# Kernel optimization log

Measured on AMD Instinct MI355X. Metric: run time of the kernel, lower is better.

The kernel has to match this reference:

```python
import jax, jax.numpy as jnp
import numpy as np

P, B, NB, NC = 256, 16, 1024, 37
L = 24  # max pairs per image == torch.mode-count for sorted im_idx (matches counts in setup_inputs)
DREL = 1936


def _linear(x, w, b):
    return x @ w.T + b


def _conv(x, w, b, stride, pad):
    y = jax.lax.conv_general_dilated(x, w, (stride, stride), [(pad, pad), (pad, pad)],
                                     dimension_numbers=('NCHW', 'OIHW', 'NCHW'))
    return y + b[None, :, None, None]


def _bn(x, g, bt, m, v):
    # eval-mode BatchNorm2d, eps=1e-5
    return g[None, :, None, None] * (x - m[None, :, None, None]) * jax.lax.rsqrt(v[None, :, None, None] + 1e-5) + bt[None, :, None, None]


def setup_inputs() -> dict:
    key = jax.random.key(0)
    ks = jax.random.split(key, 24)
    counts = np.concatenate([np.full(8, 8), np.full(8, 24)])  # sums to P=256, max = L = 24
    im_idx = jnp.asarray(np.repeat(np.arange(B), counts), dtype=jnp.int32)
    s = 0.02
    return {
        'features': jax.random.normal(ks[0], (NB, 2048), jnp.float32),
        'pair_idx': jax.random.randint(ks[1], (P, 2), 0, NB, jnp.int32),
        'im_idx': im_idx,
        'labels': jax.random.randint(ks[2], (NB,), 0, NC, jnp.int32),
        'union_feat': jax.random.normal(ks[3], (P, 1024, 7, 7), jnp.float32),
        'spatial_masks': jax.random.uniform(ks[4], (P, 2, 27, 27), jnp.float32),
        'w_union': jax.random.normal(ks[5], (256, 1024), jnp.float32) * s,
        'b_union': jnp.zeros((256,), jnp.float32),
        'conv1_w': jax.random.normal(ks[6], (128, 2, 7, 7), jnp.float32) * 0.05,
        'conv1_b': jnp.zeros((128,), jnp.float32),
        'bn1_g': jnp.ones((128,), jnp.float32),
        'bn1_b': jnp.zeros((128,), jnp.float32),
        'bn1_m': jnp.zeros((128,), jnp.float32),
        'bn1_v': jnp.ones((128,), jnp.float32),
        'conv2_w': jax.random.normal(ks[7], (256, 128, 3, 3), jnp.float32) * 0.05,
        'conv2_b': jnp.zeros((256,), jnp.float32),
        'bn2_g': jnp.ones((256,), jnp.float32),
        'bn2_b': jnp.zeros((256,), jnp.float32),
        'bn2_m': jnp.zeros((256,), jnp.float32),
        'bn2_v': jnp.ones((256,), jnp.float32),
        'subj_w': jax.random.normal(ks[8], (512, 2048), jnp.float32) * s,
        'subj_b': jnp.zeros((512,), jnp.float32),
        'obj_w': jax.random.normal(ks[9], (512, 2048), jnp.float32) * s,
        'obj_b': jnp.zeros((512,), jnp.float32),
        'vr_w': jax.random.normal(ks[10], (512, 12544), jnp.float32) * s,
        'vr_b': jnp.zeros((512,), jnp.float32),
        'emb1': jax.random.normal(ks[11], (NC, 200), jnp.float32),
        'emb2': jax.random.normal(ks[12], (NC, 200), jnp.float32),
        'bil_w': jax.random.normal(ks[13], (712, 712, 712), jnp.float32) * (1.0 / 712.0),
        'bil_b': jnp.zeros((712,), jnp.float32),
        'lin_w': jax.random.normal(ks[14], (712, 1424), jnp.float32) * s,
        'lin_b': jnp.zeros((712,), jnp.float32),
        'proj_w': jax.random.normal(ks[15], (1424, 1424), jnp.float32) * s,
        'proj_b': jnp.zeros((1424,), jnp.float32),
        'ac_w': jax.random.normal(ks[16], (157, 1936), jnp.float32) * s,
        'ac_b': jnp.zeros((157,), jnp.float32),
    }


def reference(features, pair_idx, im_idx, labels, union_feat, spatial_masks,
              w_union, b_union, conv1_w, conv1_b, bn1_g, bn1_b, bn1_m, bn1_v,
              conv2_w, conv2_b, bn2_g, bn2_b, bn2_m, bn2_v,
              subj_w, subj_b, obj_w, obj_b, vr_w, vr_b, emb1, emb2,
              bil_w, bil_b, lin_w, lin_b, proj_w, proj_b, ac_w, ac_b):
    # ragged gathers over pairs
    subj_rep = _linear(features[pair_idx[:, 0]], subj_w, subj_b)  # [P,512]
    obj_rep = _linear(features[pair_idx[:, 1]], obj_w, obj_b)    # [P,512]

    # union_func1 is a 1x1 conv -> channel contraction
    u = jnp.einsum('nchw,oc->nohw', union_feat, w_union) + b_union[None, :, None, None]
    x = jax.nn.relu(_conv(spatial_masks, conv1_w, conv1_b, 2, 3))        # [P,128,14,14]
    x = _bn(x, bn1_g, bn1_b, bn1_m, bn1_v)
    x = jax.lax.reduce_window(x, -jnp.inf, jax.lax.max, (1, 1, 3, 3), (1, 1, 2, 2),
                              ((0, 0), (0, 0), (1, 1), (1, 1)))          # [P,128,7,7]
    x = jax.nn.relu(_conv(x, conv2_w, conv2_b, 1, 1))                    # [P,256,7,7]
    x = _bn(x, bn2_g, bn2_b, bn2_m, bn2_v)
    vr = _linear((u + x).reshape(P, 256 * 49), vr_w, vr_b)               # [P,512]

    s = jnp.concatenate([subj_rep, emb1[labels[pair_idx[:, 0]]]], axis=1)  # [P,712]
    o = jnp.concatenate([obj_rep, emb2[labels[pair_idx[:, 1]]]], axis=1)   # [P,712]

    # nn.Bilinear over all pairs at once (per-row op, so the per-image loop vectorizes away)
    bil = jnp.einsum('nh,oht,nt->no', s, bil_w, o) + bil_b               # [P,712]
    z = _linear(jnp.concatenate([s, o], axis=1), lin_w, lin_b)           # [P,712]
    z = _linear(jax.nn.relu(jnp.concatenate([z, bil], axis=1)), proj_w, proj_b)  # [P,1424]
    rel = jnp.concatenate([z, vr], axis=1)                               # [P,1936]

    counts = jax.ops.segment_sum(jnp.ones((P,), jnp.int32), im_idx, num_segments=B)
    pooled = jax.ops.segment_max(rel, im_idx, num_segments=B)            # pool_type='max'
    starts = jnp.cumsum(counts) - counts
    pos = jnp.arange(P, dtype=jnp.int32) - starts[im_idx]                # position within image group
    memory = jnp.zeros((L, B, DREL), rel.dtype).at[pos, im_idx].set(rel)
    mask = (jnp.arange(L)[None, :] >= counts[:, None]).astype(jnp.uint8)  # [B,L]

    act = jax.nn.sigmoid(_linear(pooled, ac_w, ac_b))                    # [B,157]
    return act, pooled, memory, mask
```

## Files before the change

kernel.cpp:

```cpp
#include <hip/hip_runtime.h>
#include <math.h>

#define DEV __device__ __forceinline__

#define PP    256
#define BIMG  16
#define HB    712
#define KBIL  (712*712)
#define KSTEPS (KBIL/32)
#define DRELC 1936
#define BSPLIT 16
#define ZPB    991
#define KC     16
#define SLDS   520

#define SZ_ACT    (16*157)
#define OFF_ACT   0
#define OFF_POOLED (SZ_ACT)
#define SZ_POOLED (16*1936)
#define OFF_MEM   (OFF_POOLED + SZ_POOLED)
#define SZ_MEM    (24*16*1936)
#define OFF_MASK  (OFF_MEM + SZ_MEM)
#define SZ_MASK   (16*24)

#define OFF_S     0
#define OFF_O     (OFF_S + 256*712)
#define OFF_Z1    (OFF_O + 256*712)
#define OFF_BIL   (OFF_Z1 + 256*712)
#define OFF_REL   (OFF_BIL + 256*712)
#define OFF_UBUF  (OFF_REL + 256*1936)
#define OFF_XP    (OFF_UBUF + 12544*256)
#define OFF_SHARED (OFF_XP + 256*128*49)
#define OFF_X1    OFF_SHARED
#define OFF_PVR   OFF_SHARED
#define OFF_PBIL  OFF_UBUF
#define OFF_PLIN  OFF_UBUF
#define OFF_PPROJ OFF_UBUF
#define SZ_SHARED (256*128*196)
#define OFF_INTS  (OFF_SHARED + SZ_SHARED)
#define OFF_OB    (OFF_INTS + 256)
#define OFF_ST    (OFF_OB + 91136)

typedef __bf16 bf16x4 __attribute__((ext_vector_type(4)));
typedef __bf16 bf16x8 __attribute__((ext_vector_type(8)));
typedef float  f32x4  __attribute__((ext_vector_type(4)));

__global__ __launch_bounds__(256) void prep_k(const float* __restrict__ s,
    const float* __restrict__ o, __bf16* __restrict__ ob, float* __restrict__ sT) {
  int i = blockIdx.x*256 + threadIdx.x;
  if (i < 256*712) {
    ob[i] = (__bf16)o[i];
  } else {
    int j = i - 256*712;
    if (j < 712*256) {
      int h = j >> 8, n = j & 255;
      sT[j] = s[n*712 + h];
    }
  }
}

__global__ __launch_bounds__(256, 3) void bil_mfma_k(
    const __bf16* __restrict__ ob, const float* __restrict__ sT,
    const float* __restrict__ W, float* __restrict__ part) {
  __shared__ __align__(16) __bf16 Wsh[2][16*SLDS];

  const int tid = threadIdx.x;
  const int wv = tid >> 6, lane = tid & 63;
  const int lr = lane & 15, lg = lane >> 4;
  const int c0 = blockIdx.x * 16;
  const int bz = blockIdx.y;
  const int zbase = bz * ZPB;
  const int zcntT = min(ZPB, KSTEPS - zbase);
  const int nrounds = (zcntT + KC - 1) / KC;

  const int srow = tid >> 4;
  const int sl = tid & 15;
  const int scol = min(c0 + srow, 711);
  const float* wrow = W + (size_t)scol * KBIL;

  const int n0 = wv * 64;
  const int myc = c0 + lr;

  f32x4 acc[4];
  #pragma unroll
  for (int rf = 0; rf < 4; rf++) { acc[rf][0]=0.f; acc[rf][1]=0.f; acc[rf][2]=0.f; acc[rf][3]=0.f; }

  float4 st0, st1, st2, st3, st4, st5, st6, st7;
  auto stage_load = [&](int r) {
    const int kb = (zbase + r*KC) * 32 + sl*4;
    #define LD(J, DST) { int k = kb + (J)*64; if (k > KBIL-4) k = KBIL-4; \
                         DST = *(const float4*)(wrow + k); }
    LD(0, st0) LD(1, st1) LD(2, st2) LD(3, st3)
    LD(4, st4) LD(5, st5) LD(6, st6) LD(7, st7)
    #undef LD
  };
  auto stage_store = [&](int buf) {
    __bf16* base = &Wsh[buf][srow*SLDS + sl*4];
    #define ST(J, SRC) { bf16x4 b; b[0]=(__bf16)SRC.x; b[1]=(__bf16)SRC.y; \
                         b[2]=(__bf16)SRC.z; b[3]=(__bf16)SRC.w; \
                         *(bf16x4*)(base + (J)*64) = b; }
    ST(0, st0) ST(1, st1) ST(2, st2) ST(3, st3)
    ST(4, st4) ST(5, st5) ST(6, st6) ST(7, st7)
    #undef ST
  };

  stage_load(0);
  stage_store(0);
  if (nrounds > 1) stage_load(1);
  __syncthreads();

  for (int r = 0; r < nrounds; ++r) {
    const int zr0 = zbase + r*KC;
    const int zc = min(KC, zbase + zcntT - zr0);
    const int buf = r & 1;
    for (int zs = 0; zs < zc; ++zs) {
      bf16x8 b8 = *(const bf16x8*)&Wsh[buf][lr*SLDS + zs*32 + lg*8];
      const int kk = (zr0 + zs)*32 + lg*8;
      const int h = kk / 712;
      const int t = kk - h*712;
      #pragma unroll
      for (int rf = 0; rf < 4; rf++) {
        const int n = n0 + rf*16 + lr;
        bf16x8 o8 = *(const bf16x8*)&ob[(size_t)n*712 + t];
        const float sv = sT[h*256 + n];
        bf16x8 a8;
        #pragma unroll
        for (int i = 0; i < 8; i++) a8[i] = (__bf16)(sv * (float)o8[i]);
        acc[rf] = __builtin_amdgcn_mfma_f32_16x16x32_bf16(a8, b8, acc[rf], 0, 0, 0);
      }
    }
    if (r + 1 < nrounds) {
      stage_store((r+1)&1);
      __syncthreads();
      if (r + 2 < nrounds) stage_load(r+2);
    }
  }

  if (myc < 712) {
    #pragma unroll
    for (int rf = 0; rf < 4; rf++) {
      #pragma unroll
      for (int i = 0; i < 4; i++) {
        const int n = n0 + rf*16 + lg*4 + i;
        part[((size_t)bz*256 + n)*712 + myc] = acc[rf][i];
      }
    }
  }
}

struct GP {
  const float* A; const float* A2; const float* B; const float* bias;
  float* C;
  const int* gidx; int goff;
  int M, N, K;
  int ldc, coff;
  int kChunk;
  const float* bn_g; const float* bn_b; const float* bn_m; const float* bn_v;
  const float* B2; const float* bias2; float* C2;
};


template<int MODE>
DEV float loadA(const GP& p, int r, int k) {
  if (MODE == 0) { int fr = p.gidx[2*r + (int)blockIdx.z]; return p.A[fr*2048 + k]; }
  if (MODE == 2 || MODE == 8) return p.A[r*p.K + k];
  if (MODE == 3) return (k < 712) ? p.A[r*712 + k] : p.A2[r*712 + (k-712)];
  if (MODE == 4) { float v = (k < 712) ? p.A[r*712 + k] : p.A2[r*712 + (k-712)];
                   return fmaxf(v, 0.f); }
  if (MODE == 5) { int n = r/49, q = r - n*49; return p.A[(n*1024 + k)*49 + q]; }
  if (MODE == 6) {
    int n = r/49, q = r - n*49; int py = q/7, px = q - py*7;
    int ic = k/9, k9 = k - ic*9; int dy = k9/3, dx = k9 - dy*3;
    int iy = py + dy - 1, ix = px + dx - 1;
    if ((unsigned)iy >= 7u || (unsigned)ix >= 7u) return 0.f;
    return p.A[(n*128 + ic)*49 + iy*7 + ix];
  }
  return 0.f;
}

template<int MODE>
DEV float loadB(const GP& p, int c, int k) {
  if (MODE == 0) { const float* Bp = blockIdx.z ? p.B2 : p.B; return Bp[c*p.K + k]; }
  return p.B[c*p.K + k];
}

template<int MODE>
__global__ __launch_bounds__(256) void gemm_k(GP p) {
  __shared__ __align__(16) __bf16 Ash[2][64*44];
  __shared__ __align__(16) __bf16 Bsh[2][64*44];
  const int tid = threadIdx.x;
  const int srow = tid & 63, koff = (tid >> 6) * 8;
  const int col0 = blockIdx.x * 64, row0 = blockIdx.y * 64;
  const int kStart = (MODE == 0) ? 0 : blockIdx.z * p.kChunk;
  const int kEnd = min(p.K, kStart + p.kChunk);
  const int wv = tid >> 6, lane = tid & 63;
  const int lr = lane & 15, lg = lane >> 4;
  const int rh = wv >> 1, ch = wv & 1;

  f32x4 acc[2][2];
  #pragma unroll
  for (int a = 0; a < 2; a++)
    #pragma unroll
    for (int b = 0; b < 2; b++) { acc[a][b][0]=0.f; acc[a][b][1]=0.f; acc[a][b][2]=0.f; acc[a][b][3]=0.f; }

  for (int kb = kStart; kb < kEnd; kb += 32) {
    {
      const int gr = row0 + srow;
      float v[8];
      #pragma unroll
      for (int i = 0; i < 8; i++) {
        const int gk = kb + koff + i;
        v[i] = (gr < p.M && gk < kEnd) ? loadA<MODE>(p, gr, gk) : 0.f;
      }
      bf16x8 hi, lo;
      #pragma unroll
      for (int i = 0; i < 8; i++) {
        __bf16 h = (__bf16)v[i];
        hi[i] = h;
        lo[i] = (__bf16)(v[i] - (float)h);
      }
      *(bf16x8*)&Ash[0][srow*44 + koff] = hi;
      *(bf16x8*)&Ash[1][srow*44 + koff] = lo;
    }
    {
      const int gc = col0 + srow;
      float v[8];
      #pragma unroll
      for (int i = 0; i < 8; i++) {
        const int gk = kb + koff + i;
        v[i] = (gc < p.N && gk < kEnd) ? loadB<MODE>(p, gc, gk) : 0.f;
      }
      bf16x8 hi, lo;
      #pragma unroll
      for (int i = 0; i < 8; i++) {
        __bf16 h = (__bf16)v[i];
        hi[i] = h;
        lo[i] = (__bf16)(v[i] - (float)h);
      }
      *(bf16x8*)&Bsh[0][srow*44 + koff] = hi;
      *(bf16x8*)&Bsh[1][srow*44 + koff] = lo;
    }
    __syncthreads();
    #pragma unroll
    for (int rf = 0; rf < 2; rf++) {
      bf16x8 ahi = *(const bf16x8*)&Ash[0][(rh*32 + rf*16 + lr)*44 + lg*8];
      bf16x8 alo = *(const bf16x8*)&Ash[1][(rh*32 + rf*16 + lr)*44 + lg*8];
      #pragma unroll
      for (int cf = 0; cf < 2; cf++) {
        bf16x8 bhi = *(const bf16x8*)&Bsh[0][(ch*32 + cf*16 + lr)*44 + lg*8];
        bf16x8 blo = *(const bf16x8*)&Bsh[1][(ch*32 + cf*16 + lr)*44 + lg*8];
        acc[rf][cf] = __builtin_amdgcn_mfma_f32_16x16x32_bf16(ahi, bhi, acc[rf][cf], 0, 0, 0);
        acc[rf][cf] = __builtin_amdgcn_mfma_f32_16x16x32_bf16(ahi, blo, acc[rf][cf], 0, 0, 0);
        acc[rf][cf] = __builtin_amdgcn_mfma_f32_16x16x32_bf16(alo, bhi, acc[rf][cf], 0, 0, 0);
      }
    }
    __syncthreads();
  }

  #pragma unroll
  for (int rf = 0; rf < 2; rf++) {
    #pragma unroll
    for (int cf = 0; cf < 2; cf++) {
      const int c = col0 + ch*32 + cf*16 + lr;
      if (c >= p.N) continue;
      #pragma unroll
      for (int i = 0; i < 4; i++) {
        const int r = row0 + rh*32 + rf*16 + lg*4 + i;
        if (r >= p.M) continue;
        float v = acc[rf][cf][i];
        if (MODE == 2 || MODE == 3 || MODE == 4) {
          p.C[(size_t)blockIdx.z * p.M * p.N + (size_t)r * p.N + c] = v;
        } else if (MODE == 5) {
          int n = r/49, q = r - n*49;
          p.C[n*12544 + c*49 + q] = v + p.bias[c];
        } else if (MODE == 6) {
          int n = r/49, q = r - n*49;
          float sc = p.bn_g[c] / sqrtf(p.bn_v[c] + 1e-5f);
          float sh = p.bn_b[c] - p.bn_m[c]*sc;
          float t2 = fmaxf(v + p.bias[c], 0.f)*sc + sh;
          p.C[n*12544 + c*49 + q] += t2;
        } else if (MODE == 8) {
          float t2 = v + p.bias[c];
          p.C[r*p.ldc + p.coff + c] = 1.f/(1.f + expf(-t2));
        } else {
          const float* bb = blockIdx.z ? p.bias2 : p.bias;
          float* Cp = blockIdx.z ? p.C2 : p.C;
          Cp[r*p.ldc + p.coff + c] = v + bb[c];
        }
      }
    }
  }
}

__global__ __launch_bounds__(256) void reduce_k(const float* __restrict__ part,
    const float* __restrict__ bias, float* __restrict__ out,
    int S, int MN, int N, int ldc, int coff) {
  int i = blockIdx.x*256 + threadIdx.x;
  if (i >= MN) return;
  float s = 0.f;
  for (int z = 0; z < S; z++) s += part[(size_t)z*MN + i];
  int r = i / N, c = i - r*N;
  out[r*ldc + coff + c] = s + bias[c];
}

__global__ __launch_bounds__(256) void emb_k(const int* __restrict__ pi,
    const int* __restrict__ labels, const float* __restrict__ e1,
    const float* __restrict__ e2, float* __restrict__ s, float* __restrict__ o) {
  int i = blockIdx.x*256 + threadIdx.x;
  if (i >= 2*256*200) return;
  int which = i / (256*200); int rest = i - which*(256*200);
  int n = rest / 200; int j = rest - n*200;
  int lab = labels[pi[2*n + which]];
  float v = which ? e2[lab*200 + j] : e1[lab*200 + j];
  (which ? o : s)[n*712 + 512 + j] = v;
}

__global__ __launch_bounds__(256) void conv1_k(const float* __restrict__ in,
    const float* __restrict__ w, const float* __restrict__ bias,
    const float* __restrict__ g, const float* __restrict__ bt,
    const float* __restrict__ m, const float* __restrict__ vv,
    float* __restrict__ out) {
  int idx = blockIdx.x*256 + threadIdx.x;
  if (idx >= 256*128*14) return;
  int oy = idx % 14; int t = idx / 14; int c = t & 127; int n = t >> 7;
  float acc[14];
  float b0 = bias[c];
  #pragma unroll
  for (int ox = 0; ox < 14; ox++) acc[ox] = b0;
  for (int ci = 0; ci < 2; ci++) {
    #pragma unroll
    for (int ky = 0; ky < 7; ky++) {
      int iy = oy*2 - 3 + ky;
      if ((unsigned)iy >= 27u) continue;
      const float* ir = in + ((n*2 + ci)*27 + iy)*27;
      const float* wr = w + ((c*2 + ci)*7 + ky)*7;
      float iv[27];
      #pragma unroll
      for (int x = 0; x < 27; x++) iv[x] = ir[x];
      float wk[7];
      #pragma unroll
      for (int kx = 0; kx < 7; kx++) wk[kx] = wr[kx];
      #pragma unroll
      for (int kx = 0; kx < 7; kx++)
        #pragma unroll
        for (int ox = 0; ox < 14; ox++) {
          int ix = ox*2 - 3 + kx;
          if (ix >= 0 && ix < 27) acc[ox] += iv[ix]*wk[kx];
        }
    }
  }
  float sc = g[c] / sqrtf(vv[c] + 1e-5f);
  float sh = bt[c] - m[c]*sc;
  float* orow = out + ((n*128 + c)*14 + oy)*14;
  #pragma unroll
  for (int ox = 0; ox < 14; ox++) orow[ox] = fmaxf(acc[ox], 0.f)*sc + sh;
}

__global__ __launch_bounds__(256) void pool_k(const float* __restrict__ x1,
                                              float* __restrict__ xp) {
  int idx = blockIdx.x*256 + threadIdx.x;
  if (idx >= 256*128*49) return;
  int px = idx % 7; int t = idx / 7; int py = t % 7; t /= 7;
  int c = t & 127; int n = t >> 7;
  float mx = -INFINITY;
  for (int dy = 0; dy < 3; dy++) {
    int y = py*2 - 1 + dy;
    if ((unsigned)y >= 14u) continue;
    for (int dx = 0; dx < 3; dx++) {
      int x = px*2 - 1 + dx;
      if ((unsigned)x >= 14u) continue;
      mx = fmaxf(mx, x1[((n*128 + c)*14 + y)*14 + x]);
    }
  }
  xp[((n*128 + c)*7 + py)*7 + px] = mx;
}

__global__ __launch_bounds__(256) void seg_k(const int* __restrict__ im,
    int* __restrict__ counts, int* __restrict__ starts, int* __restrict__ pos) {
  __shared__ int c[16], s[16];
  int tid = threadIdx.x;
  if (tid < 16) c[tid] = 0;
  __syncthreads();
  atomicAdd(&c[im[tid]], 1);
  __syncthreads();
  if (tid == 0) { int run = 0; for (int b = 0; b < 16; b++) { s[b] = run; run += c[b]; } }
  __syncthreads();
  if (tid < 16) { counts[tid] = c[tid]; starts[tid] = s[tid]; }
  pos[tid] = tid - s[im[tid]];
}

__global__ __launch_bounds__(256) void zeromask_k(float* __restrict__ out,
                                                  const int* __restrict__ counts) {
  int i = blockIdx.x*256 + threadIdx.x;
  if (i < SZ_MEM) { out[OFF_MEM + i] = 0.f; return; }
  int j = i - SZ_MEM;
  if (j < SZ_MASK) {
    int b = j / 24, l = j - b*24;
    out[OFF_MASK + j] = (l >= counts[b]) ? 1.f : 0.f;
  }
}

__global__ __launch_bounds__(256) void scatter_k(const float* __restrict__ rel,
    const int* __restrict__ pos, const int* __restrict__ im, float* __restrict__ out) {
  int n = blockIdx.x;
  int l = pos[n], b = im[n];
  float* dst = out + OFF_MEM + ((size_t)l*16 + b)*1936;
  const float* src = rel + (size_t)n*1936;
  for (int d = threadIdx.x; d < 1936; d += 256) dst[d] = src[d];
}

__global__ __launch_bounds__(256) void pooled_k(const float* __restrict__ rel,
    const int* __restrict__ starts, const int* __restrict__ counts,
    float* __restrict__ out) {
  int b = blockIdx.y;
  int d = blockIdx.x*256 + threadIdx.x;
  if (d >= 1936) return;
  int st = starts[b], ct = counts[b];
  float mx = -INFINITY;
  for (int i = 0; i < ct; i++) mx = fmaxf(mx, rel[(size_t)(st + i)*1936 + d]);
  out[OFF_POOLED + b*1936 + d] = mx;
}

extern "C" void kernel_launch(void* const* d_in, const int* in_sizes, int n_in,
                              void* d_out, int out_size, void* d_ws, size_t ws_size,
                              hipStream_t stream) {
  const float* features   = (const float*)d_in[0];
  const int*   pair_idx   = (const int*)d_in[1];
  const int*   im_idx     = (const int*)d_in[2];
  const int*   labels     = (const int*)d_in[3];
  const float* union_feat = (const float*)d_in[4];
  const float* spatial    = (const float*)d_in[5];
  const float* w_union    = (const float*)d_in[6];
  const float* b_union    = (const float*)d_in[7];
  const float* conv1_w    = (const float*)d_in[8];
  const float* conv1_b    = (const float*)d_in[9];
  const float* bn1_g      = (const float*)d_in[10];
  const float* bn1_b      = (const float*)d_in[11];
  const float* bn1_m      = (const float*)d_in[12];
  const float* bn1_v      = (const float*)d_in[13];
  const float* conv2_w    = (const float*)d_in[14];
  const float* conv2_b    = (const float*)d_in[15];
  const float* bn2_g      = (const float*)d_in[16];
  const float* bn2_b      = (const float*)d_in[17];
  const float* bn2_m      = (const float*)d_in[18];
  const float* bn2_v      = (const float*)d_in[19];
  const float* subj_w     = (const float*)d_in[20];
  const float* subj_b     = (const float*)d_in[21];
  const float* obj_w      = (const float*)d_in[22];
  const float* obj_b      = (const float*)d_in[23];
  const float* vr_w       = (const float*)d_in[24];
  const float* vr_b       = (const float*)d_in[25];
  const float* emb1       = (const float*)d_in[26];
  const float* emb2       = (const float*)d_in[27];
  const float* bil_w      = (const float*)d_in[28];
  const float* bil_b      = (const float*)d_in[29];
  const float* lin_w      = (const float*)d_in[30];
  const float* lin_b      = (const float*)d_in[31];
  const float* proj_w     = (const float*)d_in[32];
  const float* proj_b     = (const float*)d_in[33];
  const float* ac_w       = (const float*)d_in[34];
  const float* ac_b       = (const float*)d_in[35];

  float* ws = (float*)d_ws;
  float* s_mat  = ws + OFF_S;
  float* o_mat  = ws + OFF_O;
  float* z1     = ws + OFF_Z1;
  float* bilbuf = ws + OFF_BIL;
  float* rel    = ws + OFF_REL;
  float* ubuf   = ws + OFF_UBUF;
  float* x1     = ws + OFF_X1;
  float* xp     = ws + OFF_XP;
  float* pvr    = ws + OFF_PVR;
  float* pbil   = ws + OFF_PBIL;
  float* plin   = ws + OFF_PLIN;
  float* pproj  = ws + OFF_PPROJ;
  int*   ints   = (int*)(ws + OFF_INTS);
  __bf16* obp   = (__bf16*)(ws + OFF_OB);
  float* sTp    = ws + OFF_ST;
  int* counts = ints; int* starts = ints + 16; int* pos = ints + 32;
  float* out = (float*)d_out;

  dim3 blk(256);

  {
    GP g{}; g.A = features; g.gidx = pair_idx;
    g.B = subj_w;  g.bias = subj_b;  g.C = s_mat;
    g.B2 = obj_w;  g.bias2 = obj_b;  g.C2 = o_mat;
    g.M = 256; g.N = 512; g.K = 2048; g.ldc = 712; g.coff = 0; g.kChunk = 2048;
    gemm_k<0><<<dim3(8,4,2), blk, 0, stream>>>(g);
  }
  emb_k<<<dim3(400), blk, 0, stream>>>(pair_idx, labels, emb1, emb2, s_mat, o_mat);

  {
    GP g{}; g.A = union_feat; g.B = w_union; g.bias = b_union; g.C = ubuf;
    g.M = 12544; g.N = 256; g.K = 1024; g.kChunk = 1024;
    gemm_k<5><<<dim3(4,196,1), blk, 0, stream>>>(g);
  }

  conv1_k<<<dim3(1792), blk, 0, stream>>>(spatial, conv1_w, conv1_b,
                                          bn1_g, bn1_b, bn1_m, bn1_v, x1);
  pool_k<<<dim3(6272), blk, 0, stream>>>(x1, xp);

  {
    GP g{}; g.A = xp; g.B = conv2_w; g.bias = conv2_b; g.C = ubuf;
    g.M = 12544; g.N = 256; g.K = 1152; g.kChunk = 1152;
    g.bn_g = bn2_g; g.bn_b = bn2_b; g.bn_m = bn2_m; g.bn_v = bn2_v;
    gemm_k<6><<<dim3(4,196,1), blk, 0, stream>>>(g);
  }

  {
    GP g{}; g.A = ubuf; g.B = vr_w; g.C = pvr;
    g.M = 256; g.N = 512; g.K = 12544; g.kChunk = 392;
    gemm_k<2><<<dim3(8,4,32), blk, 0, stream>>>(g);
    reduce_k<<<dim3(512), blk, 0, stream>>>(pvr, vr_b, rel, 32, 256*512, 512, 1936, 1424);
  }

  {
    GP g{}; g.A = s_mat; g.A2 = o_mat; g.B = lin_w; g.C = plin;
    g.M = 256; g.N = 712; g.K = 1424; g.kChunk = 356;
    gemm_k<3><<<dim3(12,4,4), blk, 0, stream>>>(g);
    reduce_k<<<dim3(712), blk, 0, stream>>>(plin, lin_b, z1, 4, 256*712, 712, 712, 0);
  }

  prep_k<<<dim3((256*712 + 712*256 + 255)/256), blk, 0, stream>>>(s_mat, o_mat, obp, sTp);
  bil_mfma_k<<<dim3(45, BSPLIT), blk, 0, stream>>>(obp, sTp, bil_w, pbil);
  reduce_k<<<dim3(712), blk, 0, stream>>>(pbil, bil_b, bilbuf, BSPLIT, 256*712, 712, 712, 0);

  {
    GP g{}; g.A = z1; g.A2 = bilbuf; g.B = proj_w; g.C = pproj;
    g.M = 256; g.N = 1424; g.K = 1424; g.kChunk = 712;
    gemm_k<4><<<dim3(23,4,2), blk, 0, stream>>>(g);
    reduce_k<<<dim3(1424), blk, 0, stream>>>(pproj, proj_b, rel, 2, 256*1424, 1424, 1936, 0);
  }

  seg_k<<<dim3(1), blk, 0, stream>>>(im_idx, counts, starts, pos);
  zeromask_k<<<dim3((SZ_MEM + SZ_MASK + 255)/256), blk, 0, stream>>>(out, counts);
  scatter_k<<<dim3(256), blk, 0, stream>>>(rel, pos, im_idx, out);
  pooled_k<<<dim3(8,16), blk, 0, stream>>>(rel, starts, counts, out);

  {
    GP g{}; g.A = out + OFF_POOLED; g.B = ac_w; g.bias = ac_b; g.C = out + OFF_ACT;
    g.M = 16; g.N = 157; g.K = 1936; g.ldc = 157; g.coff = 0; g.kChunk = 1936;
    gemm_k<8><<<dim3(3,1,1), blk, 0, stream>>>(g);
  }
}
```

Baseline: 2.143 ms.

## Factor bilinear by h: MFMA on o times W slice, then scale by s

The bilinear kernel is restructured to loop over h rows of the weight. For each h it runs the MFMA over t using the bf16 o matrix directly (padded to 736 columns) against the W[c,h,:] slice, then scales the per-h result by s[n,h] in fp32. This removes the per-element s*o product and bf16 conversion before every MFMA, and drops the division used to recover h and t. The split count and LDS row stride change to match the per-h tiling. The cost is more partial buffers to reduce, plus zero-padding work on each 712-wide row.

```diff
diff --git a/kernel.cpp b/kernel.cpp
--- a/kernel.cpp
+++ b/kernel.cpp
@@ -7,12 +7,11 @@
 #define BIMG  16
 #define HB    712
 #define KBIL  (712*712)
-#define KSTEPS (KBIL/32)
 #define DRELC 1936
-#define BSPLIT 16
-#define ZPB    991
-#define KC     16
-#define SLDS   520
+#define BSPLIT 24
+#define HCH    30
+#define TSTEPS 23
+#define SLDS   744
 
 #define SZ_ACT    (16*157)
 #define OFF_ACT   0
@@ -39,7 +38,7 @@
 #define SZ_SHARED (256*128*196)
 #define OFF_INTS  (OFF_SHARED + SZ_SHARED)
 #define OFF_OB    (OFF_INTS + 256)
-#define OFF_ST    (OFF_OB + 91136)
+#define OFF_ST    (OFF_OB + 94208)
 
 typedef __bf16 bf16x4 __attribute__((ext_vector_type(4)));
 typedef __bf16 bf16x8 __attribute__((ext_vector_type(8)));
@@ -48,10 +47,11 @@
 __global__ __launch_bounds__(256) void prep_k(const float* __restrict__ s,
     const float* __restrict__ o, __bf16* __restrict__ ob, float* __restrict__ sT) {
   int i = blockIdx.x*256 + threadIdx.x;
-  if (i < 256*712) {
-    ob[i] = (__bf16)o[i];
+  if (i < 256*736) {
+    int n = i / 736, t = i - n*736;
+    ob[i] = (__bf16)((t < 712) ? o[n*712 + t] : 0.f);
   } else {
-    int j = i - 256*712;
+    int j = i - 256*736;
     if (j < 712*256) {
       int h = j >> 8, n = j & 255;
       sT[j] = s[n*712 + h];
@@ -69,70 +69,77 @@
   const int lr = lane & 15, lg = lane >> 4;
   const int c0 = blockIdx.x * 16;
   const int bz = blockIdx.y;
-  const int zbase = bz * ZPB;
-  const int zcntT = min(ZPB, KSTEPS - zbase);
-  const int nrounds = (zcntT + KC - 1) / KC;
+  const int h0 = bz * HCH;
+  const int hEnd = min(712, h0 + HCH);
 
   const int srow = tid >> 4;
   const int sl = tid & 15;
-  const int scol = min(c0 + srow, 711);
-  const float* wrow = W + (size_t)scol * KBIL;
+  const bool okc = (c0 + srow) < 712;
+  const float* wrow = W + (size_t)min(c0 + srow, 711) * KBIL;
 
   const int n0 = wv * 64;
   const int myc = c0 + lr;
 
-  f32x4 acc[4];
+  f32x4 bacc[4];
   #pragma unroll
-  for (int rf = 0; rf < 4; rf++) { acc[rf][0]=0.f; acc[rf][1]=0.f; acc[rf][2]=0.f; acc[rf][3]=0.f; }
-
-  float4 st0, st1, st2, st3, st4, st5, st6, st7;
-  auto stage_load = [&](int r) {
-    const int kb = (zbase + r*KC) * 32 + sl*4;
-    #define LD(J, DST) { int k = kb + (J)*64; if (k > KBIL-4) k = KBIL-4; \
-                         DST = *(const float4*)(wrow + k); }
-    LD(0, st0) LD(1, st1) LD(2, st2) LD(3, st3)
-    LD(4, st4) LD(5, st5) LD(6, st6) LD(7, st7)
-    #undef LD
+  for (int rf = 0; rf < 4; rf++) { bacc[rf][0]=0.f; bacc[rf][1]=0.f; bacc[rf][2]=0.f; bacc[rf][3]=0.f; }
+
+  float4 stg[12];
+  auto stage_load = [&](int hh) {
+    const float* base = wrow + (size_t)hh * 712;
+    #pragma unroll
+    for (int j = 0; j < 12; j++) {
+      const int k = sl*4 + j*64;
+      if (okc && k < 712) stg[j] = *(const float4*)(base + k);
+      else stg[j] = make_float4(0.f, 0.f, 0.f, 0.f);
+    }
   };
   auto stage_store = [&](int buf) {
-    __bf16* base = &Wsh[buf][srow*SLDS + sl*4];
-    #define ST(J, SRC) { bf16x4 b; b[0]=(__bf16)SRC.x; b[1]=(__bf16)SRC.y; \
-                         b[2]=(__bf16)SRC.z; b[3]=(__bf16)SRC.w; \
-                         *(bf16x4*)(base + (J)*64) = b; }
-    ST(0, st0) ST(1, st1) ST(2, st2) ST(3, st3)
-    ST(4, st4) ST(5, st5) ST(6, st6) ST(7, st7)
-    #undef ST
+    __bf16* dst = &Wsh[buf][srow*SLDS];
+    #pragma unroll
+    for (int j = 0; j < 12; j++) {
+      const int k = sl*4 + j*64;
+      if (k < 736) {
+        bf16x4 b;
+        b[0]=(__bf16)stg[j].x; b[1]=(__bf16)stg[j].y;
+        b[2]=(__bf16)stg[j].z; b[3]=(__bf16)stg[j].w;
+        *(bf16x4*)(dst + k) = b;
+      }
+    }
   };
 
-  stage_load(0);
+  stage_load(h0);
   stage_store(0);
-  if (nrounds > 1) stage_load(1);
+  if (h0 + 1 < hEnd) stage_load(h0 + 1);
   __syncthreads();
 
-  for (int r = 0; r < nrounds; ++r) {
-    const int zr0 = zbase + r*KC;
-    const int zc = min(KC, zbase + zcntT - zr0);
-    const int buf = r & 1;
-    for (int zs = 0; zs < zc; ++zs) {
+  for (int hh = h0; hh < hEnd; ++hh) {
+    const int buf = (hh - h0) & 1;
+    f32x4 g[4];
+    #pragma unroll
+    for (int rf = 0; rf < 4; rf++) { g[rf][0]=0.f; g[rf][1]=0.f; g[rf][2]=0.f; g[rf][3]=0.f; }
+
+    #pragma unroll
+    for (int zs = 0; zs < TSTEPS; ++zs) {
       bf16x8 b8 = *(const bf16x8*)&Wsh[buf][lr*SLDS + zs*32 + lg*8];
-      const int kk = (zr0 + zs)*32 + lg*8;
-      const int h = kk / 712;
-      const int t = kk - h*712;
+      const int t0 = zs*32 + lg*8;
       #pragma unroll
       for (int rf = 0; rf < 4; rf++) {
-        const int n = n0 + rf*16 + lr;
-        bf16x8 o8 = *(const bf16x8*)&ob[(size_t)n*712 + t];
-        const float sv = sT[h*256 + n];
-        bf16x8 a8;
-        #pragma unroll
-        for (int i = 0; i < 8; i++) a8[i] = (__bf16)(sv * (float)o8[i]);
-        acc[rf] = __builtin_amdgcn_mfma_f32_16x16x32_bf16(a8, b8, acc[rf], 0, 0, 0);
-      }
-    }
-    if (r + 1 < nrounds) {
-      stage_store((r+1)&1);
+        bf16x8 o8 = *(const bf16x8*)&ob[(size_t)(n0 + rf*16 + lr)*736 + t0];
+        g[rf] = __builtin_amdgcn_mfma_f32_16x16x32_bf16(o8, b8, g[rf], 0, 0, 0);
+      }
+    }
+    #pragma unroll
+    for (int rf = 0; rf < 4; rf++) {
+      f32x4 sv = *(const f32x4*)&sT[(size_t)hh*256 + n0 + rf*16 + lg*4];
+      #pragma unroll
+      for (int i = 0; i < 4; i++) bacc[rf][i] += sv[i] * g[rf][i];
+    }
+
+    if (hh + 1 < hEnd) {
+      stage_store((hh + 1 - h0) & 1);
       __syncthreads();
-      if (r + 2 < nrounds) stage_load(r+2);
+      if (hh + 2 < hEnd) stage_load(hh + 2);
     }
   }
 
@@ -142,7 +149,7 @@
       #pragma unroll
       for (int i = 0; i < 4; i++) {
         const int n = n0 + rf*16 + lg*4 + i;
-        part[((size_t)bz*256 + n)*712 + myc] = acc[rf][i];
+        part[((size_t)bz*256 + n)*712 + myc] = bacc[rf][i];
       }
     }
   }
@@ -522,7 +529,7 @@
     reduce_k<<<dim3(712), blk, 0, stream>>>(plin, lin_b, z1, 4, 256*712, 712, 712, 0);
   }
 
-  prep_k<<<dim3((256*712 + 712*256 + 255)/256), blk, 0, stream>>>(s_mat, o_mat, obp, sTp);
+  prep_k<<<dim3((256*736 + 712*256 + 255)/256), blk, 0, stream>>>(s_mat, o_mat, obp, sTp);
   bil_mfma_k<<<dim3(45, BSPLIT), blk, 0, stream>>>(obp, sTp, bil_w, pbil);
   reduce_k<<<dim3(712), blk, 0, stream>>>(pbil, bil_b, bilbuf, BSPLIT, 256*712, 712, 712, 0);
 
```

New measurement: 3.462 ms. 61.6% more time.

## Factor bilinear s-scaling out of MFMA inner loop and prefetch o operands

Applied to the files above, without the earlier changes.

The bilinear kernel no longer scales each o fragment by s[h] before every MFMA. It accumulates raw o·W products into a per-h accumulator and multiplies by s[h] only when h changes; steps that straddle an h boundary fall back to the old per-element scaling. It also double-buffers the global loads of o fragments across k-steps to hide latency. This removes per-step conversion and multiply work and the sT load, at the cost of extra accumulator registers, branching, and slightly different bf16 rounding.

```diff
diff --git a/kernel.cpp b/kernel.cpp
--- a/kernel.cpp
+++ b/kernel.cpp
@@ -81,9 +81,13 @@
   const int n0 = wv * 64;
   const int myc = c0 + lr;
 
-  f32x4 acc[4];
+  f32x4 gacc[4], bacc[4];
   #pragma unroll
-  for (int rf = 0; rf < 4; rf++) { acc[rf][0]=0.f; acc[rf][1]=0.f; acc[rf][2]=0.f; acc[rf][3]=0.f; }
+  for (int rf = 0; rf < 4; rf++) {
+    gacc[rf][0]=0.f; gacc[rf][1]=0.f; gacc[rf][2]=0.f; gacc[rf][3]=0.f;
+    bacc[rf][0]=0.f; bacc[rf][1]=0.f; bacc[rf][2]=0.f; bacc[rf][3]=0.f;
+  }
+  int curh = (zbase * 32) / 712;
 
   float4 st0, st1, st2, st3, st4, st5, st6, st7;
   auto stage_load = [&](int r) {
@@ -104,6 +108,18 @@
     #undef ST
   };
 
+#define FLUSH() { \
+    f32x4 sv0 = *(const f32x4*)&sT[(size_t)curh*256 + n0 +  0 + lg*4]; \
+    f32x4 sv1 = *(const f32x4*)&sT[(size_t)curh*256 + n0 + 16 + lg*4]; \
+    f32x4 sv2 = *(const f32x4*)&sT[(size_t)curh*256 + n0 + 32 + lg*4]; \
+    f32x4 sv3 = *(const f32x4*)&sT[(size_t)curh*256 + n0 + 48 + lg*4]; \
+    _Pragma("unroll") \
+    for (int i_ = 0; i_ < 4; i_++) { \
+      bacc[0][i_] += sv0[i_]*gacc[0][i_]; gacc[0][i_] = 0.f; \
+      bacc[1][i_] += sv1[i_]*gacc[1][i_]; gacc[1][i_] = 0.f; \
+      bacc[2][i_] += sv2[i_]*gacc[2][i_]; gacc[2][i_] = 0.f; \
+      bacc[3][i_] += sv3[i_]*gacc[3][i_]; gacc[3][i_] = 0.f; } }
+
   stage_load(0);
   stage_store(0);
   if (nrounds > 1) stage_load(1);
@@ -113,22 +129,66 @@
     const int zr0 = zbase + r*KC;
     const int zc = min(KC, zbase + zcntT - zr0);
     const int buf = r & 1;
-    for (int zs = 0; zs < zc; ++zs) {
-      bf16x8 b8 = *(const bf16x8*)&Wsh[buf][lr*SLDS + zs*32 + lg*8];
-      const int kk = (zr0 + zs)*32 + lg*8;
-      const int h = kk / 712;
-      const int t = kk - h*712;
-      #pragma unroll
-      for (int rf = 0; rf < 4; rf++) {
-        const int n = n0 + rf*16 + lr;
-        bf16x8 o8 = *(const bf16x8*)&ob[(size_t)n*712 + t];
-        const float sv = sT[h*256 + n];
-        bf16x8 a8;
-        #pragma unroll
-        for (int i = 0; i < 8; i++) a8[i] = (__bf16)(sv * (float)o8[i]);
-        acc[rf] = __builtin_amdgcn_mfma_f32_16x16x32_bf16(a8, b8, acc[rf], 0, 0, 0);
-      }
-    }
+
+#define LOADO(ZS, O0,O1,O2,O3) { \
+      const int kk_ = (zr0 + (ZS))*32 + lg*8; \
+      const int h_ = kk_ / 712; \
+      const int t_ = kk_ - h_*712; \
+      O0 = *(const bf16x8*)&ob[(size_t)(n0 +  0 + lr)*712 + t_]; \
+      O1 = *(const bf16x8*)&ob[(size_t)(n0 + 16 + lr)*712 + t_]; \
+      O2 = *(const bf16x8*)&ob[(size_t)(n0 + 32 + lr)*712 + t_]; \
+      O3 = *(const bf16x8*)&ob[(size_t)(n0 + 48 + lr)*712 + t_]; }
+
+#define STEPX(ZS, O0,O1,O2,O3) { \
+      bf16x8 b8 = *(const bf16x8*)&Wsh[buf][lr*SLDS + (ZS)*32 + lg*8]; \
+      const int kk0_ = (zr0 + (ZS))*32; \
+      const int ha_ = kk0_ / 712; \
+      const int hb_ = (kk0_ + 31) / 712; \
+      if (ha_ == hb_) { \
+        if (ha_ != curh) { FLUSH(); curh = ha_; } \
+        gacc[0] = __builtin_amdgcn_mfma_f32_16x16x32_bf16(O0, b8, gacc[0], 0, 0, 0); \
+        gacc[1] = __builtin_amdgcn_mfma_f32_16x16x32_bf16(O1, b8, gacc[1], 0, 0, 0); \
+        gacc[2] = __builtin_amdgcn_mfma_f32_16x16x32_bf16(O2, b8, gacc[2], 0, 0, 0); \
+        gacc[3] = __builtin_amdgcn_mfma_f32_16x16x32_bf16(O3, b8, gacc[3], 0, 0, 0); \
+      } else { \
+        const int hl_ = (kk0_ + lg*8) / 712; \
+        bf16x8 a8; float sv; \
+        sv = sT[hl_*256 + n0 +  0 + lr]; \
+        _Pragma("unroll") for (int i_=0;i_<8;i_++) a8[i_]=(__bf16)(sv*(float)O0[i_]); \
+        bacc[0] = __builtin_amdgcn_mfma_f32_16x16x32_bf16(a8, b8, bacc[0], 0, 0, 0); \
+        sv = sT[hl_*256 + n0 + 16 + lr]; \
+        _Pragma("unroll") for (int i_=0;i_<8;i_++) a8[i_]=(__bf16)(sv*(float)O1[i_]); \
+        bacc[1] = __builtin_amdgcn_mfma_f32_16x16x32_bf16(a8, b8, bacc[1], 0, 0, 0); \
+        sv = sT[hl_*256 + n0 + 32 + lr]; \
+        _Pragma("unroll") for (int i_=0;i_<8;i_++) a8[i_]=(__bf16)(sv*(float)O2[i_]); \
+        bacc[2] = __builtin_amdgcn_mfma_f32_16x16x32_bf16(a8, b8, bacc[2], 0, 0, 0); \
+        sv = sT[hl_*256 + n0 + 48 + lr]; \
+        _Pragma("unroll") for (int i_=0;i_<8;i_++) a8[i_]=(__bf16)(sv*(float)O3[i_]); \
+        bacc[3] = __builtin_amdgcn_mfma_f32_16x16x32_bf16(a8, b8, bacc[3], 0, 0, 0); \
+      } }
+
+    if (zc == KC) {
+      bf16x8 pA0, pA1, pA2, pA3, pB0, pB1, pB2, pB3;
+      LOADO(0, pA0,pA1,pA2,pA3)
+      LOADO(1, pB0,pB1,pB2,pB3)
+      for (int zs = 0; zs + 3 < KC; zs += 2) {
+        STEPX(zs,   pA0,pA1,pA2,pA3)
+        LOADO(zs+2, pA0,pA1,pA2,pA3)
+        STEPX(zs+1, pB0,pB1,pB2,pB3)
+        LOADO(zs+3, pB0,pB1,pB2,pB3)
+      }
+      STEPX(KC-2, pA0,pA1,pA2,pA3)
+      STEPX(KC-1, pB0,pB1,pB2,pB3)
+    } else {
+      for (int zs = 0; zs < zc; ++zs) {
+        bf16x8 t0, t1, t2, t3;
+        LOADO(zs, t0,t1,t2,t3)
+        STEPX(zs, t0,t1,t2,t3)
+      }
+    }
+#undef LOADO
+#undef STEPX
+
     if (r + 1 < nrounds) {
       stage_store((r+1)&1);
       __syncthreads();
@@ -136,13 +196,16 @@
     }
   }
 
+  FLUSH();
+#undef FLUSH
+
   if (myc < 712) {
     #pragma unroll
     for (int rf = 0; rf < 4; rf++) {
       #pragma unroll
       for (int i = 0; i < 4; i++) {
         const int n = n0 + rf*16 + lg*4 + i;
-        part[((size_t)bz*256 + n)*712 + myc] = acc[rf][i];
+        part[((size_t)bz*256 + n)*712 + myc] = bacc[rf][i];
       }
     }
   }
```

New measurement: 2.697 ms. 25.8% more time.
